# Optimization experiments

Hardware: AMD Instinct MI355X
Metric: run time of the kernel (lower is better)

## Reference

```python
import jax, jax.numpy as jnp
import numpy as np

N = 100000   # nodes
E = 1600000  # edges (avg degree 16)
IN, HID, OUT = 128, 128, 64


def setup_inputs() -> dict:
    key = jax.random.key(0)
    k = jax.random.split(key, 6)
    feat = jax.random.normal(k[0], (N, IN), dtype=jnp.float32)
    src = jax.random.randint(k[1], (E,), 0, N)
    dst = jax.random.randint(k[2], (E,), 0, N)
    W1 = jax.random.normal(k[3], (IN, HID), dtype=jnp.float32) * (1.0 / np.sqrt(IN))
    b1 = jnp.zeros((HID,), dtype=jnp.float32)
    W2 = jax.random.normal(k[4], (HID, OUT), dtype=jnp.float32) * (1.0 / np.sqrt(HID))
    b2 = jnp.zeros((OUT,), dtype=jnp.float32)
    return {"feat": feat, "src": src, "dst": dst, "W1": W1, "b1": b1, "W2": W2, "b2": b2}


def _graph_conv(x, src, dst, c_src, c_dst, W, b):
    # DGL GraphConv, norm='both': D_dst^{-1/2} A (D_src^{-1/2} X W) + b
    # Apply W before the edge gather (mathematically identical, less edge traffic).
    h = (x * c_src[:, None]) @ W                      # [N, out]
    m = jax.ops.segment_sum(h[src], dst, num_segments=N)  # SpMM aggregate
    return m * c_dst[:, None] + b


def reference(feat, src, dst, W1, b1, W2, b2):
    ones = jnp.ones((src.shape[0],), dtype=feat.dtype)
    out_deg = jax.ops.segment_sum(ones, src, num_segments=N)
    in_deg = jax.ops.segment_sum(ones, dst, num_segments=N)
    c_src = jnp.clip(out_deg, 1.0, None) ** -0.5
    c_dst = jnp.clip(in_deg, 1.0, None) ** -0.5
    h = jax.nn.relu(_graph_conv(feat, src, dst, c_src, c_dst, W1, b1))
    h = _graph_conv(h, src, dst, c_src, c_dst, W2, b2)
    # dgl.mean_nodes over a single graph -> [1, OUT]
    return jnp.mean(h, axis=0, keepdims=True)
```

## Files before the change

### kernel.cpp

```cpp
#include <hip/hip_runtime.h>
#include <hip/hip_bf16.h>

#define FD 128
#define OD 64
#define SLOT 64
#define MAXNB 512
#define CHUNK 4096
#define NSLAB 64

typedef __hip_bfloat16 bf16;
typedef unsigned int u32;
typedef unsigned short u16;
typedef unsigned char u8;
typedef __attribute__((ext_vector_type(8))) short short8;
typedef __attribute__((ext_vector_type(4))) float f32x4;
typedef __attribute__((ext_vector_type(2))) float f32x2;

__device__ __forceinline__ float ldf(const float* p, size_t i) { return p[i]; }
__device__ __forceinline__ float ldf(const bf16* p, size_t i) { return __bfloat162float(p[i]); }
__device__ __forceinline__ float us2f(u16 u) {
    union { float f; u32 i; } w; w.i = ((u32)u) << 16; return w.f;
}
__device__ __forceinline__ u16 f2us(float f) {
    bf16 h = __float2bfloat16(f);
    return *reinterpret_cast<u16*>(&h);
}

__device__ __forceinline__ u32 f8e(float x) {
    union { float f; u32 i; } w; w.f = x;
    u32 s = (w.i >> 24) & 0x80u;
    float a = fabsf(x);
    if (a < 0.015625f) {
        u32 m = (u32)(int)rintf(a * 512.0f);
        return s | m;
    }
    if (a > 448.0f) a = 448.0f;
    w.f = a;
    u32 mag = w.i + 0x7FFFFu + ((w.i >> 20) & 1u);
    if (mag > 0x43E00000u) mag = 0x43E00000u;
    u32 e8 = (mag >> 23) - 120u;
    u32 m3 = (mag >> 20) & 7u;
    return s | (e8 << 3) | m3;
}
__device__ __forceinline__ float f8d(u32 b) {
    float v;
    if ((b & 0x78u) == 0u) {
        v = (float)(b & 7u) * 0x1p-9f;
    } else {
        union { u32 i; float f; } w;
        w.i = ((b & 0x7Fu) << 20) + 0x3C000000u;
        v = w.f;
    }
    return (b & 0x80u) ? -v : v;
}

__device__ __forceinline__ u32 sniff(const u16* __restrict__ w1raw, u32* shflag) {
    if (threadIdx.x < 64) {
        int insane = 0;
        for (int i = threadIdx.x; i < 128; i += 64) {
            unsigned e = (w1raw[i] >> 7) & 0xFF;
            if (e != 0 && (e < 100 || e > 140)) insane++;
        }
        for (int o = 32; o > 0; o >>= 1) insane += __shfl_down(insane, o);
        if (threadIdx.x == 0) *shflag = (insane > 16) ? 1u : 0u;
    }
    __syncthreads();
    return *shflag;
}

__global__ __launch_bounds__(1024) void k_hw(const int* __restrict__ src,
                                             const int* __restrict__ dst,
                                             const u16* __restrict__ w1raw,
                                             const void* __restrict__ W1, const void* __restrict__ b1,
                                             u16* __restrict__ W1T, float* __restrict__ b1f,
                                             u32* __restrict__ cmT_d, u32* __restrict__ cmT_s,
                                             int E, int NB) {
    __shared__ u32 smem[1024];
    __shared__ u32 flsh;
    int t = threadIdx.x, blk = blockIdx.x, G = gridDim.x;
    u32 fl = sniff(w1raw, &flsh);

    for (long i = (long)blk * 1024 + t; i < FD * FD; i += (long)G * 1024) {
        int nn = (int)(i >> 7), k = (int)(i & 127);
        W1T[i] = fl ? f2us(ldf((const float*)W1, (size_t)k * FD + nn))
                    : f2us(ldf((const bf16*)W1, (size_t)k * FD + nn));
    }
    if (blk == 0 && t < FD)
        b1f[t] = fl ? ldf((const float*)b1, t) : ldf((const bf16*)b1, t);

    u32* hd = smem;
    u32* hs = smem + 512;
    for (int i = t; i < NB; i += 1024) { hd[i] = 0; hs[i] = 0; }
    __syncthreads();
    long e0 = (long)blk * CHUNK;
    #pragma unroll
    for (int k = 0; k < CHUNK / 1024; k++) {
        long e = e0 + t + 1024L * k;
        if (e < E) {
            atomicAdd(&hd[((u32)dst[e]) >> 8], 1u);
            atomicAdd(&hs[((u32)src[e]) >> 8], 1u);
        }
    }
    __syncthreads();
    for (int i = t; i < NB; i += 1024) {
        cmT_d[(size_t)blk * NB + i] = hd[i];
        cmT_s[(size_t)blk * NB + i] = hs[i];
    }
}

__global__ __launch_bounds__(1024) void k_colpre(u32* __restrict__ cmT_d, u32* __restrict__ cmT_s,
                                                 u32* __restrict__ totd, u32* __restrict__ tots,
                                                 int NB, int nchunk) {
    __shared__ u32 sS[1024];
    int bb = blockIdx.x;
    u32* cm  = (bb < NB) ? cmT_d : cmT_s;
    u32* tot = (bb < NB) ? totd : tots;
    int b = (bb < NB) ? bb : bb - NB;
    int t = threadIdx.x;
    u32 carry = 0;
    for (int c0 = 0; c0 < nchunk; c0 += 1024) {
        int c = c0 + t;
        u32 v = (c < nchunk) ? cm[(size_t)c * NB + b] : 0u;
        sS[t] = v;
        __syncthreads();
        for (int o = 1; o < 1024; o <<= 1) {
            u32 x = (t >= o) ? sS[t - o] : 0u;
            __syncthreads();
            sS[t] += x;
            __syncthreads();
        }
        if (c < nchunk) cm[(size_t)c * NB + b] = carry + sS[t] - v;
        u32 bt = sS[1023];
        __syncthreads();
        carry += bt;
    }
    if (t == 0) tot[b] = carry;
}

__global__ void k_scanB(const u32* __restrict__ totd, const u32* __restrict__ tots,
                        u32* __restrict__ bstart_d, u32* __restrict__ bstart_s,
                        float* __restrict__ accum_slab, int NB) {
    __shared__ u32 ts[1024];
    const u32* h = blockIdx.x ? tots : totd;
    u32* bs = blockIdx.x ? bstart_s : bstart_d;
    int t = threadIdx.x;
    for (int i = blockIdx.x * 4096 + t; i < (blockIdx.x + 1) * 4096; i += 1024)
        accum_slab[i] = 0.0f;
    u32 v = (t < NB) ? h[t] : 0u;
    ts[t] = v;
    __syncthreads();
    for (int o = 1; o < 1024; o <<= 1) {
        u32 x = (t >= o) ? ts[t - o] : 0u;
        __syncthreads();
        ts[t] += x;
        __syncthreads();
    }
    if (t < NB) bs[t] = ts[t] - v;
}

__global__ __launch_bounds__(1024) void k_scat(const int* __restrict__ src,
                                               const int* __restrict__ dst,
                                               const u32* __restrict__ cmT_d,
                                               const u32* __restrict__ cmT_s,
                                               const u32* __restrict__ bstart_d,
                                               const u32* __restrict__ bstart_s,
                                               u32* __restrict__ pairs, u32* __restrict__ srcb,
                                               int E, int NB) {
    __shared__ u32 hd[MAXNB], hs[MAXNB];
    __shared__ u32 baseD[MAXNB], baseS[MAXNB];
    int t = threadIdx.x, blk = blockIdx.x;
    for (int i = t; i < NB; i += 1024) {
        hd[i] = 0; hs[i] = 0;
        baseD[i] = cmT_d[(size_t)blk * NB + i] + bstart_d[i];
        baseS[i] = cmT_s[(size_t)blk * NB + i] + bstart_s[i];
    }
    __syncthreads();
    long e0 = (long)blk * CHUNK;
    #pragma unroll
    for (int k = 0; k < CHUNK / 1024; k++) {
        long e = e0 + t + 1024L * k;
        if (e < E) {
            u32 s = (u32)src[e], d = (u32)dst[e];
            u32 rd = atomicAdd(&hd[d >> 8], 1u);
            u32 rs = atomicAdd(&hs[s >> 8], 1u);
            pairs[baseD[d >> 8] + rd] = ((d & 255u) << 24) | s;
            srcb [baseS[s >> 8] + rs] = ((s & 255u) << 24) | d;
        }
    }
}

__global__ __launch_bounds__(1024) void k_csr(const u32* __restrict__ pairs,
                                              const u32* __restrict__ bstart,
                                              const u32* __restrict__ bhist, u32* __restrict__ col,
                                              u32* __restrict__ cnt_d, float* __restrict__ c_dst,
                                              int N) {
    __shared__ u32 lc[256];
    int b = blockIdx.x, t = threadIdx.x;
    if (t < 256) lc[t] = 0;
    __syncthreads();
    u32 s0 = bstart[b], c = bhist[b];
    for (u32 i = t; i < c; i += 1024) {
        u32 pk = pairs[s0 + i];
        u32 local = pk >> 24;
        u32 r = atomicAdd(&lc[local], 1u);
        if (r < SLOT) col[(((size_t)b * 256 + local) << 6) + r] = pk & 0xFFFFFFu;
    }
    __syncthreads();
    if (t < 256) {
        int node = b * 256 + t;
        if (node < N) {
            cnt_d[node] = lc[t];
            c_dst[node] = rsqrtf(fmaxf((float)lc[t], 1.0f));
        }
    }
}

__global__ __launch_bounds__(1024) void k_cwf8(const u32* __restrict__ srcb,
                                               const u32* __restrict__ bstart,
                                               const u32* __restrict__ bhist,
                                               const float* __restrict__ c_dst,
                                               float* __restrict__ c_src, float* __restrict__ wprod,
                                               const u16* __restrict__ w1raw,
                                               const void* __restrict__ feat,
                                               u32* __restrict__ f8w, int N) {
    __shared__ u32 lc[256];
    __shared__ float accF[256];
    __shared__ float csl[256];
    __shared__ u32 flsh;
    int b = blockIdx.x, t = threadIdx.x;
    u32 fl = sniff(w1raw, &flsh);
    if (t < 256) { lc[t] = 0; accF[t] = 0.0f; }
    __syncthreads();
    u32 s0 = bstart[b], c = bhist[b];
    for (u32 i = t; i < c; i += 1024) {
        u32 pk = srcb[s0 + i];
        atomicAdd(&lc[pk >> 24], 1u);
        atomicAdd(&accF[pk >> 24], c_dst[pk & 0xFFFFFFu]);
    }
    __syncthreads();
    if (t < 256) {
        int node = b * 256 + t;
        float cs = 0.0f;
        if (node < N) {
            cs = rsqrtf(fmaxf((float)lc[t], 1.0f));
            c_src[node] = cs;
            wprod[node] = accF[t] * cs;
        }
        csl[t] = cs;
    }
    __syncthreads();
    for (int wi = t; wi < 256 * 32; wi += 1024) {
        int row = wi >> 5;
        int node = b * 256 + row;
        if (node >= N) continue;
        float cs = csl[row];
        size_t b0 = (size_t)node * FD + (size_t)(wi & 31) * 4;
        u32 pk;
        if (fl == 0u) {
            const bf16* f = (const bf16*)feat;
            pk = f8e(cs * ldf(f, b0))       | (f8e(cs * ldf(f, b0 + 1)) << 8)
               | (f8e(cs * ldf(f, b0 + 2)) << 16) | (f8e(cs * ldf(f, b0 + 3)) << 24);
        } else {
            const float* f = (const float*)feat;
            pk = f8e(cs * ldf(f, b0))       | (f8e(cs * ldf(f, b0 + 1)) << 8)
               | (f8e(cs * ldf(f, b0 + 2)) << 16) | (f8e(cs * ldf(f, b0 + 3)) << 24);
        }
        f8w[(size_t)node * 32 + (wi & 31)] = pk;
    }
    if (b == 0 && t < 32) f8w[(size_t)N * 32 + t] = 0u;
}

__global__ __launch_bounds__(256) void k_layer1a(const u8* __restrict__ f8,
                                                 const u16* __restrict__ W1T,
                                                 const float* __restrict__ b1f,
                                                 const float* __restrict__ c_dst,
                                                 const unsigned* __restrict__ cnt_d,
                                                 const unsigned* __restrict__ col,
                                                 const float* __restrict__ wprod,
                                                 float* __restrict__ accum_slab, int n) {
    __shared__ __align__(16) u16 xsb[64 * 144];
    __shared__ float b1l[FD];
    __shared__ float cdl[64], wpl[64];
    __shared__ unsigned degl[64];
    int t = threadIdx.x;
    int base = blockIdx.x * 64;

    if (t < FD) b1l[t] = b1f[t];
    if (t < 64) {
        int rr = base + t;
        unsigned cd = (rr < n) ? cnt_d[rr] : 0u;
        cdl[t] = (rr < n) ? c_dst[rr] : 0.0f;
        wpl[t] = (rr < n) ? wprod[rr] : 0.0f;
        degl[t] = (cd < SLOT) ? cd : SLOT;
    }
    __syncthreads();

    int w = __builtin_amdgcn_readfirstlane(t >> 6);
    int l = t & 63;
    int m0 = w * 16;
    int q = l >> 4, lm = l & 15;
    int j0 = l * 2;
    unsigned zrow = (unsigned)n;

    for (int g = 0; g < 16; g++) {
        int loc = m0 + g;
        int node = base + loc;
        unsigned degv = degl[loc];
        size_t cb = ((size_t)node) << 6;
        float acc0 = 0.0f, acc1 = 0.0f;
        for (unsigned qq = 0; qq < degv; qq += 16) {
            unsigned lim = degv - qq;
            const unsigned* cp = col + cb + qq;
            uint4 P0 = *(const uint4*)(cp);
            uint4 P1 = *(const uint4*)(cp + 4);
            uint4 P2 = *(const uint4*)(cp + 8);
            uint4 P3 = *(const uint4*)(cp + 12);
            unsigned raw[16] = {P0.x, P0.y, P0.z, P0.w, P1.x, P1.y, P1.z, P1.w,
                                P2.x, P2.y, P2.z, P2.w, P3.x, P3.y, P3.z, P3.w};
            #pragma unroll
            for (int k = 0; k < 16; k++) {
                unsigned sk = __builtin_amdgcn_readfirstlane(raw[k]);
                sk = ((unsigned)k < lim) ? sk : zrow;
                u32 v = (u32)*(const u16*)(f8 + (((size_t)sk) << 7) + j0);
#if __has_builtin(__builtin_amdgcn_cvt_pk_f32_fp8)
                f32x2 dd = __builtin_amdgcn_cvt_pk_f32_fp8((int)v, false);
                acc0 += dd[0];
                acc1 += dd[1];
#else
                acc0 += f8d(v & 0xFFu);
                acc1 += f8d(v >> 8);
#endif
            }
        }
        u32 pk = ((u32)f2us(acc1) << 16) | (u32)f2us(acc0);
        *(u32*)&xsb[loc * 144 + j0] = pk;
    }

    short8 af[4];
    #pragma unroll
    for (int s = 0; s < 4; s++)
        af[s] = *(const short8*)&xsb[(m0 + lm) * 144 + s * 32 + q * 8];
    __syncthreads();
    float* part = (float*)xsb;

    #pragma unroll 1
    for (int h2 = 0; h2 < 2; h2++) {
        #pragma unroll 1
        for (int tt = 0; tt < 4; tt++) {
            int nglob = h2 * 64 + tt * 16 + lm;
            f32x4 c = {0.0f, 0.0f, 0.0f, 0.0f};
            #pragma unroll
            for (int s = 0; s < 4; s++) {
                short8 bfr = *(const short8*)&W1T[(size_t)nglob * FD + s * 32 + q * 8];
                c = __builtin_amdgcn_mfma_f32_16x16x32_bf16(af[s], bfr, c, 0, 0, 0);
            }
            float bb = b1l[nglob];
            float ps = 0.0f;
            #pragma unroll
            for (int r = 0; r < 4; r++) {
                int loc = m0 + q * 4 + r;
                float hv = fmaxf(c[r] * cdl[loc] + bb, 0.0f);
                ps += wpl[loc] * hv;
            }
            ps += __shfl_down(ps, 32);
            ps += __shfl_down(ps, 16);
            if (l < 16) part[w * FD + nglob] = ps;
        }
    }
    __syncthreads();
    if (t < FD) {
        float v = part[0 * FD + t] + part[1 * FD + t] + part[2 * FD + t] + part[3 * FD + t];
        unsafeAtomicAdd(&accum_slab[(blockIdx.x & (NSLAB - 1)) * FD + t], v);
    }
}

__global__ void k_finalF(const u16* __restrict__ w1raw,
                         const float* __restrict__ accum_slab,
                         const void* __restrict__ W2, const void* __restrict__ b2v,
                         void* __restrict__ out, float invN) {
    __shared__ float a128[FD];
    __shared__ u32 flsh;
    u32 fl = sniff(w1raw, &flsh);
    int t = threadIdx.x;
    float s = 0.0f;
    for (int r = 0; r < NSLAB; r++) s += accum_slab[r * FD + t];
    a128[t] = s;
    __syncthreads();
    if (t < OD) {
        float acc = 0.0f;
        if (fl == 0u) {
            const bf16* w = (const bf16*)W2;
            for (int k = 0; k < FD; k++) acc += a128[k] * ldf(w, (size_t)k * OD + t);
            ((bf16*)out)[t] = __float2bfloat16(acc * invN + ldf((const bf16*)b2v, t));
        } else {
            const float* w = (const float*)W2;
            for (int k = 0; k < FD; k++) acc += a128[k] * ldf(w, (size_t)k * OD + t);
            ((float*)out)[t] = acc * invN + ldf((const float*)b2v, t);
        }
    }
}

extern "C" void kernel_launch(void* const* d_in, const int* in_sizes, int n_in,
                              void* d_out, int out_size, void* d_ws, size_t ws_size,
                              hipStream_t stream) {
    const int* src = (const int*)d_in[1];
    const int* dst = (const int*)d_in[2];
    int N = in_sizes[0] / FD;
    int E = in_sizes[1];
    int NB = (N + 255) >> 8;
    int nchunk = (E + CHUNK - 1) / CHUNK;

    char* ws = (char*)d_ws;
    size_t o = 0;
    auto take = [&](size_t bytes) { size_t r = o; o = (o + bytes + 255) & ~(size_t)255; return r; };
    float*    accum_slab = (float*) (ws + take((size_t)NSLAB * FD * 4));
    u32*      totd     = (u32*)     (ws + take((size_t)NB * 4));
    u32*      tots     = (u32*)     (ws + take((size_t)NB * 4));
    u32*      bstart_d = (u32*)     (ws + take((size_t)NB * 4));
    u32*      bstart_s = (u32*)     (ws + take((size_t)NB * 4));
    float*    wprod    = (float*)   (ws + take((size_t)N * 4));
    float*    c_src    = (float*)   (ws + take((size_t)N * 4));
    float*    c_dst    = (float*)   (ws + take((size_t)N * 4));
    unsigned* cnt_d    = (unsigned*)(ws + take((size_t)N * 4));
    u16*      W1T      = (u16*)     (ws + take(FD * FD * 2));
    float*    b1f      = (float*)   (ws + take(FD * 4));
    u32*      cmT_d    = (u32*)     (ws + take((size_t)NB * nchunk * 4));
    u32*      cmT_s    = (u32*)     (ws + take((size_t)NB * nchunk * 4));
    u32*      pairs    = (u32*)     (ws + take((size_t)E * 4));
    u32*      srcb     = (u32*)     (ws + take((size_t)E * 4));
    u32*      col      = (u32*)     (ws + take((size_t)N * SLOT * 4));
    u8*       f8       = (u8*)      (ws + take(((size_t)N + 1) * FD));

    const u16* w1raw = (const u16*)d_in[3];

    k_hw<<<nchunk, 1024, 0, stream>>>(src, dst, w1raw, d_in[3], d_in[4], W1T, b1f,
                                      cmT_d, cmT_s, E, NB);
    k_colpre<<<2 * NB, 1024, 0, stream>>>(cmT_d, cmT_s, totd, tots, NB, nchunk);
    k_scanB<<<2, 1024, 0, stream>>>(totd, tots, bstart_d, bstart_s, accum_slab, NB);
    k_scat<<<nchunk, 1024, 0, stream>>>(src, dst, cmT_d, cmT_s, bstart_d, bstart_s,
                                        pairs, srcb, E, NB);
    k_csr<<<NB, 1024, 0, stream>>>(pairs, bstart_d, totd, col, cnt_d, c_dst, N);
    k_cwf8<<<NB, 1024, 0, stream>>>(srcb, bstart_s, tots, c_dst, c_src, wprod,
                                    w1raw, d_in[0], (u32*)f8, N);

    int gl1 = (N + 63) / 64;
    k_layer1a<<<gl1, 256, 0, stream>>>(f8, W1T, b1f, c_dst, cnt_d, col, wprod, accum_slab, N);

    float invN = 1.0f / (float)N;
    k_finalF<<<1, 128, 0, stream>>>(w1raw, accum_slab, d_in[5], d_in[6], d_out, invN);
}
```

Before: 240.7 us.

## Fold bucket scan into scatter, split CSR/degree and feature-quantize kernels across more blocks

Drops the separate two-block k_scanB launch. Its accum_slab zeroing moves into k_colpre, and every k_scat block now redundantly computes the bucket-start prefix sums. The dst-CSR build and the src-degree count run as two halves of one 2*NB-block kernel. The c_dst-weighted wprod sum and the fp8 feature quantization become two independent halves of another 2*NB-block kernel, so the feature pass no longer waits behind the per-bucket atomic loop in the same block. This saves one launch and roughly doubles block-level parallelism in the preprocessing stages. In exchange each scatter block does two redundant scans, and the srcb buffer is read twice.

```diff
diff --git a/kernel.cpp b/kernel.cpp
--- a/kernel.cpp
+++ b/kernel.cpp
@@ -110,13 +110,15 @@
 
 __global__ __launch_bounds__(1024) void k_colpre(u32* __restrict__ cmT_d, u32* __restrict__ cmT_s,
                                                  u32* __restrict__ totd, u32* __restrict__ tots,
+                                                 float* __restrict__ accum_slab,
                                                  int NB, int nchunk) {
     __shared__ u32 sS[1024];
-    int bb = blockIdx.x;
+    int bb = blockIdx.x, t = threadIdx.x;
+    for (long i = (long)bb * 1024 + t; i < NSLAB * FD; i += (long)gridDim.x * 1024)
+        accum_slab[i] = 0.0f;
     u32* cm  = (bb < NB) ? cmT_d : cmT_s;
     u32* tot = (bb < NB) ? totd : tots;
     int b = (bb < NB) ? bb : bb - NB;
-    int t = threadIdx.x;
     u32 carry = 0;
     for (int c0 = 0; c0 < nchunk; c0 += 1024) {
         int c = c0 + t;
@@ -137,42 +139,48 @@
     if (t == 0) tot[b] = carry;
 }
 
-__global__ void k_scanB(const u32* __restrict__ totd, const u32* __restrict__ tots,
-                        u32* __restrict__ bstart_d, u32* __restrict__ bstart_s,
-                        float* __restrict__ accum_slab, int NB) {
-    __shared__ u32 ts[1024];
-    const u32* h = blockIdx.x ? tots : totd;
-    u32* bs = blockIdx.x ? bstart_s : bstart_d;
-    int t = threadIdx.x;
-    for (int i = blockIdx.x * 4096 + t; i < (blockIdx.x + 1) * 4096; i += 1024)
-        accum_slab[i] = 0.0f;
-    u32 v = (t < NB) ? h[t] : 0u;
-    ts[t] = v;
-    __syncthreads();
-    for (int o = 1; o < 1024; o <<= 1) {
-        u32 x = (t >= o) ? ts[t - o] : 0u;
-        __syncthreads();
-        ts[t] += x;
-        __syncthreads();
-    }
-    if (t < NB) bs[t] = ts[t] - v;
-}
-
 __global__ __launch_bounds__(1024) void k_scat(const int* __restrict__ src,
                                                const int* __restrict__ dst,
                                                const u32* __restrict__ cmT_d,
                                                const u32* __restrict__ cmT_s,
-                                               const u32* __restrict__ bstart_d,
-                                               const u32* __restrict__ bstart_s,
+                                               const u32* __restrict__ totd,
+                                               const u32* __restrict__ tots,
+                                               u32* __restrict__ bstart_d, u32* __restrict__ bstart_s,
                                                u32* __restrict__ pairs, u32* __restrict__ srcb,
                                                int E, int NB) {
     __shared__ u32 hd[MAXNB], hs[MAXNB];
-    __shared__ u32 baseD[MAXNB], baseS[MAXNB];
+    __shared__ u32 bD[MAXNB], bS[MAXNB];
+    __shared__ u32 sS[MAXNB];
     int t = threadIdx.x, blk = blockIdx.x;
+
+    u32 v = (t < NB) ? totd[t] : 0u;
+    if (t < MAXNB) sS[t] = v;
+    __syncthreads();
+    for (int o = 1; o < MAXNB; o <<= 1) {
+        u32 x = (t >= o && t < MAXNB) ? sS[t - o] : 0u;
+        __syncthreads();
+        if (t < MAXNB) sS[t] += x;
+        __syncthreads();
+    }
+    if (t < NB) bD[t] = sS[t] - v;
+    __syncthreads();
+    u32 v2 = (t < NB) ? tots[t] : 0u;
+    if (t < MAXNB) sS[t] = v2;
+    __syncthreads();
+    for (int o = 1; o < MAXNB; o <<= 1) {
+        u32 x = (t >= o && t < MAXNB) ? sS[t - o] : 0u;
+        __syncthreads();
+        if (t < MAXNB) sS[t] += x;
+        __syncthreads();
+    }
+    if (t < NB) bS[t] = sS[t] - v2;
+    if (blk == 0 && t < NB) { bstart_d[t] = bD[t]; bstart_s[t] = bS[t]; }
+    __syncthreads();
+
     for (int i = t; i < NB; i += 1024) {
         hd[i] = 0; hs[i] = 0;
-        baseD[i] = cmT_d[(size_t)blk * NB + i] + bstart_d[i];
-        baseS[i] = cmT_s[(size_t)blk * NB + i] + bstart_s[i];
+        bD[i] += cmT_d[(size_t)blk * NB + i];
+        bS[i] += cmT_s[(size_t)blk * NB + i];
     }
     __syncthreads();
     long e0 = (long)blk * CHUNK;
@@ -183,91 +191,110 @@
             u32 s = (u32)src[e], d = (u32)dst[e];
             u32 rd = atomicAdd(&hd[d >> 8], 1u);
             u32 rs = atomicAdd(&hs[s >> 8], 1u);
-            pairs[baseD[d >> 8] + rd] = ((d & 255u) << 24) | s;
-            srcb [baseS[s >> 8] + rs] = ((s & 255u) << 24) | d;
-        }
-    }
-}
-
-__global__ __launch_bounds__(1024) void k_csr(const u32* __restrict__ pairs,
-                                              const u32* __restrict__ bstart,
-                                              const u32* __restrict__ bhist, u32* __restrict__ col,
-                                              u32* __restrict__ cnt_d, float* __restrict__ c_dst,
-                                              int N) {
+            pairs[bD[d >> 8] + rd] = ((d & 255u) << 24) | s;
+            srcb [bS[s >> 8] + rs] = ((s & 255u) << 24) | d;
+        }
+    }
+}
+
+__global__ __launch_bounds__(1024) void k_csrcs(const u32* __restrict__ pairs,
+                                                const u32* __restrict__ srcb,
+                                                const u32* __restrict__ bstart_d,
+                                                const u32* __restrict__ bstart_s,
+                                                const u32* __restrict__ totd,
+                                                const u32* __restrict__ tots,
+                                                u32* __restrict__ col,
+                                                u32* __restrict__ cnt_d, float* __restrict__ c_dst,
+                                                float* __restrict__ c_src, int N, int NB) {
     __shared__ u32 lc[256];
-    int b = blockIdx.x, t = threadIdx.x;
+    int b0 = blockIdx.x, t = threadIdx.x;
     if (t < 256) lc[t] = 0;
     __syncthreads();
-    u32 s0 = bstart[b], c = bhist[b];
-    for (u32 i = t; i < c; i += 1024) {
-        u32 pk = pairs[s0 + i];
-        u32 local = pk >> 24;
-        u32 r = atomicAdd(&lc[local], 1u);
-        if (r < SLOT) col[(((size_t)b * 256 + local) << 6) + r] = pk & 0xFFFFFFu;
-    }
-    __syncthreads();
-    if (t < 256) {
-        int node = b * 256 + t;
-        if (node < N) {
-            cnt_d[node] = lc[t];
-            c_dst[node] = rsqrtf(fmaxf((float)lc[t], 1.0f));
-        }
-    }
-}
-
-__global__ __launch_bounds__(1024) void k_cwf8(const u32* __restrict__ srcb,
-                                               const u32* __restrict__ bstart,
-                                               const u32* __restrict__ bhist,
-                                               const float* __restrict__ c_dst,
-                                               float* __restrict__ c_src, float* __restrict__ wprod,
-                                               const u16* __restrict__ w1raw,
-                                               const void* __restrict__ feat,
-                                               u32* __restrict__ f8w, int N) {
-    __shared__ u32 lc[256];
-    __shared__ float accF[256];
-    __shared__ float csl[256];
-    __shared__ u32 flsh;
-    int b = blockIdx.x, t = threadIdx.x;
-    u32 fl = sniff(w1raw, &flsh);
-    if (t < 256) { lc[t] = 0; accF[t] = 0.0f; }
-    __syncthreads();
-    u32 s0 = bstart[b], c = bhist[b];
-    for (u32 i = t; i < c; i += 1024) {
-        u32 pk = srcb[s0 + i];
-        atomicAdd(&lc[pk >> 24], 1u);
-        atomicAdd(&accF[pk >> 24], c_dst[pk & 0xFFFFFFu]);
-    }
-    __syncthreads();
-    if (t < 256) {
-        int node = b * 256 + t;
-        float cs = 0.0f;
-        if (node < N) {
-            cs = rsqrtf(fmaxf((float)lc[t], 1.0f));
-            c_src[node] = cs;
-            wprod[node] = accF[t] * cs;
-        }
-        csl[t] = cs;
-    }
-    __syncthreads();
-    for (int wi = t; wi < 256 * 32; wi += 1024) {
-        int row = wi >> 5;
-        int node = b * 256 + row;
-        if (node >= N) continue;
-        float cs = csl[row];
-        size_t b0 = (size_t)node * FD + (size_t)(wi & 31) * 4;
-        u32 pk;
-        if (fl == 0u) {
-            const bf16* f = (const bf16*)feat;
-            pk = f8e(cs * ldf(f, b0))       | (f8e(cs * ldf(f, b0 + 1)) << 8)
-               | (f8e(cs * ldf(f, b0 + 2)) << 16) | (f8e(cs * ldf(f, b0 + 3)) << 24);
-        } else {
-            const float* f = (const float*)feat;
-            pk = f8e(cs * ldf(f, b0))       | (f8e(cs * ldf(f, b0 + 1)) << 8)
-               | (f8e(cs * ldf(f, b0 + 2)) << 16) | (f8e(cs * ldf(f, b0 + 3)) << 24);
-        }
-        f8w[(size_t)node * 32 + (wi & 31)] = pk;
-    }
-    if (b == 0 && t < 32) f8w[(size_t)N * 32 + t] = 0u;
+    if (b0 < NB) {
+        int b = b0;
+        u32 s0 = bstart_d[b], c = totd[b];
+        for (u32 i = t; i < c; i += 1024) {
+            u32 pk = pairs[s0 + i];
+            u32 local = pk >> 24;
+            u32 r = atomicAdd(&lc[local], 1u);
+            if (r < SLOT) col[(((size_t)b * 256 + local) << 6) + r] = pk & 0xFFFFFFu;
+        }
+        __syncthreads();
+        if (t < 256) {
+            int node = b * 256 + t;
+            if (node < N) {
+                cnt_d[node] = lc[t];
+                c_dst[node] = rsqrtf(fmaxf((float)lc[t], 1.0f));
+            }
+        }
+    } else {
+        int b = b0 - NB;
+        u32 s0 = bstart_s[b], c = tots[b];
+        for (u32 i = t; i < c; i += 1024)
+            atomicAdd(&lc[srcb[s0 + i] >> 24], 1u);
+        __syncthreads();
+        if (t < 256) {
+            int node = b * 256 + t;
+            if (node < N) c_src[node] = rsqrtf(fmaxf((float)lc[t], 1.0f));
+        }
+    }
+}
+
+__global__ __launch_bounds__(1024) void k_wf8(const u32* __restrict__ srcb,
+                                              const u32* __restrict__ bstart_s,
+                                              const u32* __restrict__ tots,
+                                              const float* __restrict__ c_dst,
+                                              const float* __restrict__ c_src,
+                                              float* __restrict__ wprod,
+                                              const u16* __restrict__ w1raw,
+                                              const void* __restrict__ feat,
+                                              u32* __restrict__ f8w, int N, int NB) {
+    int b0 = blockIdx.x, t = threadIdx.x;
+    if (b0 < NB) {
+        __shared__ float accF[256];
+        int b = b0;
+        if (t < 256) accF[t] = 0.0f;
+        __syncthreads();
+        u32 s0 = bstart_s[b], c = tots[b];
+        for (u32 i = t; i < c; i += 1024) {
+            u32 pk = srcb[s0 + i];
+            atomicAdd(&accF[pk >> 24], c_dst[pk & 0xFFFFFFu]);
+        }
+        __syncthreads();
+        if (t < 256) {
+            int node = b * 256 + t;
+            if (node < N) wprod[node] = accF[t] * c_src[node];
+        }
+    } else {
+        __shared__ float csl[256];
+        __shared__ u32 flsh;
+        u32 fl = sniff(w1raw, &flsh);
+        int b = b0 - NB;
+        if (t < 256) {
+            int node = b * 256 + t;
+            csl[t] = (node < N) ? c_src[node] : 0.0f;
+        }
+        __syncthreads();
+        for (int wi = t; wi < 256 * 32; wi += 1024) {
+            int row = wi >> 5;
+            int node = b * 256 + row;
+            if (node >= N) continue;
+            float cs = csl[row];
+            size_t p0 = (size_t)node * FD + (size_t)(wi & 31) * 4;
+            u32 pk;
+            if (fl == 0u) {
+                const bf16* f = (const bf16*)feat;
+                pk = f8e(cs * ldf(f, p0))       | (f8e(cs * ldf(f, p0 + 1)) << 8)
+                   | (f8e(cs * ldf(f, p0 + 2)) << 16) | (f8e(cs * ldf(f, p0 + 3)) << 24);
+            } else {
+                const float* f = (const float*)feat;
+                pk = f8e(cs * ldf(f, p0))       | (f8e(cs * ldf(f, p0 + 1)) << 8)
+                   | (f8e(cs * ldf(f, p0 + 2)) << 16) | (f8e(cs * ldf(f, p0 + 3)) << 24);
+            }
+            f8w[(size_t)node * 32 + (wi & 31)] = pk;
+        }
+        if (b == 0 && t < 32) f8w[(size_t)N * 32 + t] = 0u;
+    }
 }
 
 __global__ __launch_bounds__(256) void k_layer1a(const u8* __restrict__ f8,
@@ -435,13 +462,13 @@
 
     k_hw<<<nchunk, 1024, 0, stream>>>(src, dst, w1raw, d_in[3], d_in[4], W1T, b1f,
                                       cmT_d, cmT_s, E, NB);
-    k_colpre<<<2 * NB, 1024, 0, stream>>>(cmT_d, cmT_s, totd, tots, NB, nchunk);
-    k_scanB<<<2, 1024, 0, stream>>>(totd, tots, bstart_d, bstart_s, accum_slab, NB);
-    k_scat<<<nchunk, 1024, 0, stream>>>(src, dst, cmT_d, cmT_s, bstart_d, bstart_s,
-                                        pairs, srcb, E, NB);
-    k_csr<<<NB, 1024, 0, stream>>>(pairs, bstart_d, totd, col, cnt_d, c_dst, N);
-    k_cwf8<<<NB, 1024, 0, stream>>>(srcb, bstart_s, tots, c_dst, c_src, wprod,
-                                    w1raw, d_in[0], (u32*)f8, N);
+    k_colpre<<<2 * NB, 1024, 0, stream>>>(cmT_d, cmT_s, totd, tots, accum_slab, NB, nchunk);
+    k_scat<<<nchunk, 1024, 0, stream>>>(src, dst, cmT_d, cmT_s, totd, tots,
+                                        bstart_d, bstart_s, pairs, srcb, E, NB);
+    k_csrcs<<<2 * NB, 1024, 0, stream>>>(pairs, srcb, bstart_d, bstart_s, totd, tots,
+                                         col, cnt_d, c_dst, c_src, N, NB);
+    k_wf8<<<2 * NB, 1024, 0, stream>>>(srcb, bstart_s, tots, c_dst, c_src, wprod,
+                                       w1raw, d_in[0], (u32*)f8, N, NB);
 
     int gl1 = (N + 63) / 64;
     k_layer1a<<<gl1, 256, 0, stream>>>(f8, W1T, b1f, c_dst, cnt_d, col, wprod, accum_slab, N);
```

Result: no change. 238.6 us (-0.9%).
